# Kernel tuning notes

Hardware: AMD Instinct MI355X
Metric: run time of the kernel (lower is better)

Reference implementation:

```python
import jax, jax.numpy as jnp
import numpy as np

B, L, D = 2, 2048, 1024
H = 16
HD = D // H  # 64


def setup_inputs() -> dict:
    key = jax.random.key(0)
    ks = jax.random.split(key, 7)
    s = 0.02
    return {
        "x": jax.random.normal(ks[0], (B, L, D), dtype=jnp.float32),
        "Wq": jax.random.normal(ks[1], (D, D), dtype=jnp.float32) * s,
        "bq": jnp.zeros((D,), dtype=jnp.float32),
        "Wkv": jax.random.normal(ks[2], (D, 2 * D), dtype=jnp.float32) * s,
        "bkv": jnp.zeros((2 * D,), dtype=jnp.float32),
        "Wo": jax.random.normal(ks[3], (D, D), dtype=jnp.float32) * s,
        "bo": jnp.zeros((D,), dtype=jnp.float32),
    }


def reference(x, Wq, bq, Wkv, bkv, Wo, bo):
    # q/kv projections (self-attention: key/value come from x)
    q = x @ Wq + bq                      # [B, L, D]
    kv = x @ Wkv + bkv                   # [B, L, 2D]
    k, v = jnp.split(kv, 2, axis=-1)     # each [B, L, D]
    # split heads: 'b l (h c) -> b h l c' (rope_embed_fraction=0 -> RoPE is identity)
    def heads(t):
        return t.reshape(B, L, H, HD).transpose(0, 2, 1, 3)
    qh, kh, vh = heads(q), heads(k), heads(v)   # [B, H, L, HD]
    scale = 1.0 / jnp.sqrt(jnp.asarray(HD, dtype=x.dtype))
    scores = jnp.einsum('bhqc,bhkc->bhqk', qh, kh) * scale  # [B, H, L, L]
    attn = jax.nn.softmax(scores, axis=-1)
    y = jnp.einsum('bhqk,bhkc->bhqc', attn, vh)             # [B, H, L, HD]
    # merge heads: 'b h l c -> b l (h c)'
    y = y.transpose(0, 2, 1, 3).reshape(B, L, D)
    return (y @ Wo + bo).reshape(x.shape)
```

## Files before the change

kernel.cpp:

```cpp
#include <hip/hip_runtime.h>

#define B_  2
#define L_  2048
#define D_  1024
#define H_  16
#define HD_ 64

typedef __attribute__((ext_vector_type(8))) short bf16x8;
typedef __attribute__((ext_vector_type(4))) float f32x4;

#define MFMA16(a, b, c) __builtin_amdgcn_mfma_f32_16x16x32_bf16(a, b, c, 0, 0, 0)

__device__ __forceinline__ unsigned short f2bf(float f) {
    union { float f; unsigned u; } v; v.f = f;
    unsigned r = v.u + 0x7FFFu + ((v.u >> 16) & 1u);
    return (unsigned short)(r >> 16);
}

__global__ __launch_bounds__(256) void convert_bf16(
    const float* __restrict__ in, unsigned short* __restrict__ out, int n4)
{
    for (int i = blockIdx.x * blockDim.x + threadIdx.x; i < n4;
         i += gridDim.x * blockDim.x) {
        float4 v = *(const float4*)(in + (size_t)i * 4);
        ushort4 u;
        u.x = f2bf(v.x); u.y = f2bf(v.y); u.z = f2bf(v.z); u.w = f2bf(v.w);
        *(ushort4*)(out + (size_t)i * 4) = u;
    }
}

__global__ __launch_bounds__(256) void prep_w(
    const float* __restrict__ Wq, const float* __restrict__ Wkv,
    const float* __restrict__ Wo,
    unsigned short* __restrict__ Wqt, unsigned short* __restrict__ Wkvt,
    unsigned short* __restrict__ Wot)
{
    __shared__ float t[32][33];
    const int z = blockIdx.z;
    const float* W;  unsigned short* Wt;  int N, nc;
    if (z == 0)      { W = Wq;  Wt = Wqt;  N = 1024; nc = 0; }
    else if (z == 1) { W = Wo;  Wt = Wot;  N = 1024; nc = 0; }
    else             { W = Wkv; Wt = Wkvt; N = 2048; nc = (z - 2) * 1024; }
    const int tx = threadIdx.x & 31, ty = threadIdx.x >> 5;
    const int n0 = nc + blockIdx.x * 32, k0 = blockIdx.y * 32;
    #pragma unroll
    for (int r = 0; r < 4; ++r)
        t[ty + r * 8][tx] = W[(size_t)(k0 + ty + r * 8) * N + n0 + tx];
    __syncthreads();
    #pragma unroll
    for (int r = 0; r < 4; ++r)
        Wt[(size_t)(n0 + ty + r * 8) * 1024 + k0 + tx] = f2bf(t[tx][ty + r * 8]);
}

__global__ __launch_bounds__(512, 1) void gemm_qkv8(
    const unsigned short* __restrict__ A,
    const unsigned short* __restrict__ Bt,
    const float* __restrict__ bq, const float* __restrict__ bkv,
    unsigned short* __restrict__ Qb, unsigned short* __restrict__ Kb,
    unsigned short* __restrict__ Vtg, float qscl)
{
    const int KDIM = 1024, NT = 16;
    __shared__ __align__(16) unsigned short lds[65536];

    const int tid = threadIdx.x;
    const int w = tid >> 6, l = tid & 63, g = l >> 4, ln = l & 15;
    const int wm = (w >> 2) & 1, wn = w & 3;

    const int lin = blockIdx.x;
    const int wg = (lin & 7) * 24 + (lin >> 3);
    const int by = wg / 12, bx = wg % 12;
    const int m0 = by * 256, n0 = bx * 256;

    const int sr8 = w * 8 + (l >> 3);
    const int sc  = (l & 7) ^ ((l >> 3) & 7);
    const unsigned short* Asrc = A  + (size_t)m0 * KDIM + sc * 8;
    const unsigned short* Bsrc = Bt + (size_t)n0 * KDIM + sc * 8;

#define SLOT_A(d, h) (lds + ((d) * 2 + (h)) * 8192)
#define SLOT_B(d, h) (lds + 32768 + ((d) * 2 + (h)) * 8192)

#define STG(slotp, srcp, hh, kt_) do {                                        \
    _Pragma("unroll")                                                         \
    for (int r_ = 0; r_ < 2; ++r_) {                                          \
        const int row_ = (hh) * 128 + r_ * 64 + sr8;                          \
        __builtin_amdgcn_global_load_lds(                                     \
            (const __attribute__((address_space(1))) void*)                   \
                ((srcp) + (size_t)row_ * KDIM + (kt_) * 64),                  \
            (__attribute__((address_space(3))) void*)                         \
                ((slotp) + r_ * 4096 + w * 512 + l * 8),                      \
            16, 0, 0);                                                        \
    }                                                                         \
} while (0)

    f32x4 acc[8][4];
    #pragma unroll
    for (int i = 0; i < 8; ++i)
        #pragma unroll
        for (int j = 0; j < 4; ++j) acc[i][j] = (f32x4){0.f, 0.f, 0.f, 0.f};

    bf16x8 aR[4][2], bB0[2][2], bB1[2][2];

    STG(SLOT_A(0, 0), Asrc, 0, 0);
    STG(SLOT_B(0, 1), Bsrc, 1, 0);
    STG(SLOT_A(0, 1), Asrc, 1, 0);
    STG(SLOT_B(0, 0), Bsrc, 0, 0);
    STG(SLOT_A(1, 0), Asrc, 0, 1);
    STG(SLOT_B(1, 1), Bsrc, 1, 1);

    #pragma unroll 1
    for (int kt = 0; kt < NT; ++kt) {
        const int cur = kt & 1, nxt = cur ^ 1;
        asm volatile("s_waitcnt vmcnt(4)" ::: "memory");
        __builtin_amdgcn_s_barrier();

        #pragma unroll
        for (int mi = 0; mi < 4; ++mi)
            #pragma unroll
            for (int kc = 0; kc < 2; ++kc) {
                const int rho = wm * 64 + mi * 16 + ln, c = kc * 4 + g;
                aR[mi][kc] = *(const bf16x8*)
                    (SLOT_A(cur, 0) + rho * 64 + ((c ^ (rho & 7)) * 8));
            }
        #pragma unroll
        for (int ni = 0; ni < 2; ++ni)
            #pragma unroll
            for (int kc = 0; kc < 2; ++kc) {
                const int rho = wn * 32 + ni * 16 + ln, c = kc * 4 + g;
                bB0[ni][kc] = *(const bf16x8*)
                    (SLOT_B(cur, 0) + rho * 64 + ((c ^ (rho & 7)) * 8));
            }
        if (kt + 1 < NT) STG(SLOT_A(nxt, 1), Asrc, 1, kt + 1);
        __builtin_amdgcn_s_barrier();
        asm volatile("s_waitcnt lgkmcnt(0)" ::: "memory");
        __builtin_amdgcn_s_setprio(1);
        #pragma unroll
        for (int mi = 0; mi < 4; ++mi)
            #pragma unroll
            for (int ni = 0; ni < 2; ++ni) {
                acc[mi][ni] = MFMA16(aR[mi][0], bB0[ni][0], acc[mi][ni]);
                acc[mi][ni] = MFMA16(aR[mi][1], bB0[ni][1], acc[mi][ni]);
            }
        __builtin_amdgcn_s_setprio(0);
        __builtin_amdgcn_s_barrier();

        #pragma unroll
        for (int ni = 0; ni < 2; ++ni)
            #pragma unroll
            for (int kc = 0; kc < 2; ++kc) {
                const int rho = wn * 32 + ni * 16 + ln, c = kc * 4 + g;
                bB1[ni][kc] = *(const bf16x8*)
                    (SLOT_B(cur, 1) + rho * 64 + ((c ^ (rho & 7)) * 8));
            }
        if (kt + 1 < NT) STG(SLOT_B(nxt, 0), Bsrc, 0, kt + 1);
        __builtin_amdgcn_s_barrier();
        asm volatile("s_waitcnt lgkmcnt(0)" ::: "memory");
        __builtin_amdgcn_s_setprio(1);
        #pragma unroll
        for (int mi = 0; mi < 4; ++mi)
            #pragma unroll
            for (int ni = 0; ni < 2; ++ni) {
                acc[mi][2 + ni] = MFMA16(aR[mi][0], bB1[ni][0], acc[mi][2 + ni]);
                acc[mi][2 + ni] = MFMA16(aR[mi][1], bB1[ni][1], acc[mi][2 + ni]);
            }
        __builtin_amdgcn_s_setprio(0);
        __builtin_amdgcn_s_barrier();

        #pragma unroll
        for (int mi = 0; mi < 4; ++mi)
            #pragma unroll
            for (int kc = 0; kc < 2; ++kc) {
                const int rho = wm * 64 + mi * 16 + ln, c = kc * 4 + g;
                aR[mi][kc] = *(const bf16x8*)
                    (SLOT_A(cur, 1) + rho * 64 + ((c ^ (rho & 7)) * 8));
            }
        if (kt + 2 < NT) STG(SLOT_A(cur, 0), Asrc, 0, kt + 2);
        __builtin_amdgcn_s_barrier();
        asm volatile("s_waitcnt lgkmcnt(0)" ::: "memory");
        __builtin_amdgcn_s_setprio(1);
        #pragma unroll
        for (int mi = 0; mi < 4; ++mi)
            #pragma unroll
            for (int ni = 0; ni < 2; ++ni) {
                acc[4 + mi][2 + ni] = MFMA16(aR[mi][0], bB1[ni][0], acc[4 + mi][2 + ni]);
                acc[4 + mi][2 + ni] = MFMA16(aR[mi][1], bB1[ni][1], acc[4 + mi][2 + ni]);
            }
        __builtin_amdgcn_s_setprio(0);
        __builtin_amdgcn_s_barrier();

        if (kt + 2 < NT) STG(SLOT_B(cur, 1), Bsrc, 1, kt + 2);
        __builtin_amdgcn_s_barrier();
        __builtin_amdgcn_s_setprio(1);
        #pragma unroll
        for (int mi = 0; mi < 4; ++mi)
            #pragma unroll
            for (int ni = 0; ni < 2; ++ni) {
                acc[4 + mi][ni] = MFMA16(aR[mi][0], bB0[ni][0], acc[4 + mi][ni]);
                acc[4 + mi][ni] = MFMA16(aR[mi][1], bB0[ni][1], acc[4 + mi][ni]);
            }
        __builtin_amdgcn_s_setprio(0);
        __builtin_amdgcn_s_barrier();
    }
#undef STG
#undef SLOT_A
#undef SLOT_B

    const int region = n0 >> 10;
    if (region == 2) {
        #pragma unroll
        for (int nh = 0; nh < 2; ++nh)
            #pragma unroll
            for (int ni = 0; ni < 2; ++ni) {
                const int d = n0 - 2048 + nh * 128 + wn * 32 + ni * 16 + ln;
                const float bv = bkv[1024 + d];
                #pragma unroll
                for (int mh = 0; mh < 2; ++mh)
                    #pragma unroll
                    for (int mi = 0; mi < 4; ++mi) {
                        const int tok = m0 + mh * 128 + wm * 64 + mi * 16 + g * 4;
                        const int bb = tok >> 11, t4 = tok & 2047;
                        const f32x4 av = acc[mh * 4 + mi][nh * 2 + ni];
                        ushort4 p4;
                        p4.x = f2bf(av[0] + bv); p4.y = f2bf(av[1] + bv);
                        p4.z = f2bf(av[2] + bv); p4.w = f2bf(av[3] + bv);
                        *(ushort4*)(Vtg + ((size_t)bb * 1024 + d) * 2048 + t4) = p4;
                    }
            }
    } else {
        const int isQ = (region == 0);
        const float osc = isQ ? qscl : 1.f;
        #pragma unroll
        for (int nh = 0; nh < 2; ++nh)
            #pragma unroll
            for (int ni = 0; ni < 2; ++ni) {
                const int col = n0 + nh * 128 + wn * 32 + ni * 16 + ln;
                const float bv = isQ ? bq[col] : bkv[col - 1024];
                const int ck = isQ ? col : col - 1024;
                #pragma unroll
                for (int mh = 0; mh < 2; ++mh)
                    #pragma unroll
                    for (int mi = 0; mi < 4; ++mi) {
                        const int row = m0 + mh * 128 + wm * 64 + mi * 16 + g * 4;
                        const f32x4 av = acc[mh * 4 + mi][nh * 2 + ni];
                        #pragma unroll
                        for (int r = 0; r < 4; ++r) {
                            const float vout = (av[r] + bv) * osc;
                            if (isQ)
                                Qb[(size_t)(row + r) * 1024 + ck] = f2bf(vout);
                            else
                                Kb[(size_t)(row + r) * 1024 + ck] = f2bf(vout);
                        }
                    }
            }
    }
}

__global__ __launch_bounds__(256) void gemm_bt(
    const unsigned short* __restrict__ A,
    const unsigned short* __restrict__ Bt,
    const float* __restrict__ bias,
    float* __restrict__ Cout, int M, int N, int K)
{
    __shared__ __align__(16) unsigned short As[128 * 32];
    __shared__ __align__(16) unsigned short Bs[128 * 32];
    const int tid = threadIdx.x;
    const int w = tid >> 6, l = tid & 63, g = l >> 4, ln = l & 15;
    const int wm = w >> 1, wn = w & 1;
    const int m0 = blockIdx.y * 128, n0 = blockIdx.x * 128;

    f32x4 acc[4][4];
    #pragma unroll
    for (int i = 0; i < 4; ++i)
        #pragma unroll
        for (int j = 0; j < 4; ++j) acc[i][j] = (f32x4){0.f, 0.f, 0.f, 0.f};

    const char* Ab = (const char*)A;
    const char* Bb = (const char*)Bt;
    const size_t strideK = (size_t)K * 2;

    for (int k0 = 0; k0 < K; k0 += 32) {
        #pragma unroll
        for (int i = 0; i < 2; ++i) {
            const int b = w * 2048 + i * 1024 + l * 16;
            const int row = b >> 6, cb = b & 63;
            __builtin_amdgcn_global_load_lds(
                (const __attribute__((address_space(1))) void*)
                    (Ab + (size_t)(m0 + row) * strideK + (size_t)k0 * 2 + cb),
                (__attribute__((address_space(3))) void*)
                    ((char*)As + w * 2048 + i * 1024),
                16, 0, 0);
            __builtin_amdgcn_global_load_lds(
                (const __attribute__((address_space(1))) void*)
                    (Bb + (size_t)(n0 + row) * strideK + (size_t)k0 * 2 + cb),
                (__attribute__((address_space(3))) void*)
                    ((char*)Bs + w * 2048 + i * 1024),
                16, 0, 0);
        }
        __syncthreads();
        bf16x8 af[4], bfr[4];
        #pragma unroll
        for (int m = 0; m < 4; ++m)
            af[m] = *(const bf16x8*)(As + (wm * 64 + m * 16 + ln) * 32 + g * 8);
        #pragma unroll
        for (int n = 0; n < 4; ++n)
            bfr[n] = *(const bf16x8*)(Bs + (wn * 64 + n * 16 + ln) * 32 + g * 8);
        #pragma unroll
        for (int m = 0; m < 4; ++m)
            #pragma unroll
            for (int n = 0; n < 4; ++n)
                acc[m][n] = MFMA16(af[m], bfr[n], acc[m][n]);
        __syncthreads();
    }

    #pragma unroll
    for (int n = 0; n < 4; ++n) {
        const int col = n0 + wn * 64 + n * 16 + ln;
        const float bv = bias[col];
        #pragma unroll
        for (int m = 0; m < 4; ++m) {
            const int row = m0 + wm * 64 + m * 16 + g * 4;
            #pragma unroll
            for (int r = 0; r < 4; ++r)
                Cout[(size_t)(row + r) * N + col] = acc[m][n][r] + bv;
        }
    }
}

__global__ __launch_bounds__(256) void attn_mfma(
    const unsigned short* __restrict__ Qb,
    const unsigned short* __restrict__ Kb,
    const unsigned short* __restrict__ Vtg,
    unsigned short* __restrict__ Yb)
{
    __shared__ __align__(16) unsigned short Ks[2][64 * 64];
    __shared__ __align__(16) unsigned short Vs[2][64 * 64];
    __shared__ __align__(16) unsigned short Pl[4][32 * 64];

    const int tid = threadIdx.x;
    const int w = tid >> 6, l = tid & 63, g = l >> 4, ln = l & 15;
    const int dd = blockIdx.x;
    const int bid = (dd & 7) * 64 + (dd >> 3);
    const int qc = bid & 15, h = (bid >> 4) & 15, b = bid >> 8;
    const int qrow = b * L_ + qc * 128 + w * 32;

    const int sub = l >> 3;
    const int scc = (l & 7) ^ sub;
    const unsigned short* ksrc = Kb  + (size_t)(b * L_) * 1024 + h * HD_ + scc * 8;
    const unsigned short* vsrc = Vtg + (size_t)(b * D_ + h * HD_) * 2048 + scc * 8;

#define STAGE(jj, bb) do {                                                    \
    _Pragma("unroll")                                                         \
    for (int i_ = 0; i_ < 2; ++i_) {                                          \
        const int rowK = w * 16 + i_ * 8 + sub;                               \
        __builtin_amdgcn_global_load_lds(                                     \
            (const __attribute__((address_space(1))) void*)                   \
                (ksrc + (size_t)((jj) * 64 + rowK) * 1024),                   \
            (__attribute__((address_space(3))) void*)                         \
                (&Ks[bb][w * 1024 + i_ * 512]), 16, 0, 0);                    \
        __builtin_amdgcn_global_load_lds(                                     \
            (const __attribute__((address_space(1))) void*)                   \
                (vsrc + (size_t)rowK * 2048 + (jj) * 64),                     \
            (__attribute__((address_space(3))) void*)                         \
                (&Vs[bb][w * 1024 + i_ * 512]), 16, 0, 0);                    \
    }                                                                         \
} while (0)

    bf16x8 qa[2][2];
    #pragma unroll
    for (int qt = 0; qt < 2; ++qt)
        #pragma unroll
        for (int c = 0; c < 2; ++c)
            qa[qt][c] = *(const bf16x8*)
                (Qb + (size_t)(qrow + qt * 16 + ln) * D_ + h * HD_ + c * 32 + g * 8);

    f32x4 o[2][4], lacc[2];
    #pragma unroll
    for (int qt = 0; qt < 2; ++qt) {
        #pragma unroll
        for (int dt = 0; dt < 4; ++dt) o[qt][dt] = (f32x4){0.f, 0.f, 0.f, 0.f};
        lacc[qt] = (f32x4){0.f, 0.f, 0.f, 0.f};
    }
    const short one_s = (short)0x3F80;
    const bf16x8 ones = {one_s, one_s, one_s, one_s, one_s, one_s, one_s, one_s};

    unsigned short* Pw = &Pl[w][0];
    const int swzl = (ln & 7) << 3;
    const int swp  = (ln & 7) << 1;

#define ATT_BODY(BUF, TNEXT, NBUF, DOSTG) do {                                \
    if (DOSTG) STAGE(TNEXT, NBUF);                                            \
    const unsigned short* Kc = &Ks[BUF][0];                                   \
    const unsigned short* Vc = &Vs[BUF][0];                                   \
    bf16x8 kb[4][2];                                                          \
    _Pragma("unroll")                                                         \
    for (int kt = 0; kt < 4; ++kt)                                            \
        _Pragma("unroll")                                                     \
        for (int c = 0; c < 2; ++c)                                           \
            kb[kt][c] = *(const bf16x8*)                                      \
                (Kc + (kt * 16 + ln) * 64 + ((c * 32 + g * 8) ^ swzl));       \
    f32x4 s[2][4];                                                            \
    const f32x4 z = (f32x4){0.f, 0.f, 0.f, 0.f};                              \
    __builtin_amdgcn_s_setprio(1);                                            \
    _Pragma("unroll")                                                         \
    for (int qt = 0; qt < 2; ++qt)                                            \
        _Pragma("unroll")                                                     \
        for (int kt = 0; kt < 4; ++kt) {                                      \
            f32x4 t0 = MFMA16(kb[kt][0], qa[qt][0], z);                       \
            s[qt][kt] = MFMA16(kb[kt][1], qa[qt][1], t0);                     \
        }                                                                     \
    __builtin_amdgcn_s_setprio(0);                                            \
    _Pragma("unroll")                                                         \
    for (int qt = 0; qt < 2; ++qt) {                                          \
        const int prow = (qt * 16 + ln) * 64;                                 \
        _Pragma("unroll")                                                     \
        for (int kt = 0; kt < 4; ++kt) {                                      \
            union { float f; unsigned u; } c0, c1, c2u, c3;                   \
            c0.f = __builtin_exp2f(s[qt][kt][0]);                             \
            c1.f = __builtin_exp2f(s[qt][kt][1]);                             \
            c2u.f = __builtin_exp2f(s[qt][kt][2]);                            \
            c3.f = __builtin_exp2f(s[qt][kt][3]);                             \
            uint2 pk;                                                         \
            pk.x = __builtin_amdgcn_perm(c1.u, c0.u, 0x07060302u);            \
            pk.y = __builtin_amdgcn_perm(c3.u, c2u.u, 0x07060302u);           \
            *(uint2*)(Pw + prow + (((kt * 4 + g) ^ swp) << 2)) = pk;          \
        }                                                                     \
    }                                                                         \
    bf16x8 pa[2][2], vb[4][2];                                                \
    _Pragma("unroll")                                                         \
    for (int qt = 0; qt < 2; ++qt)                                            \
        _Pragma("unroll")                                                     \
        for (int c2 = 0; c2 < 2; ++c2)                                        \
            pa[qt][c2] = *(const bf16x8*)                                     \
                (Pw + (qt * 16 + ln) * 64 + (((c2 * 8 + g * 2) ^ swp) << 2)); \
    _Pragma("unroll")                                                         \
    for (int dt = 0; dt < 4; ++dt)                                            \
        _Pragma("unroll")                                                     \
        for (int c2 = 0; c2 < 2; ++c2)                                        \
            vb[dt][c2] = *(const bf16x8*)                                     \
                (Vc + (dt * 16 + ln) * 64 + ((c2 * 32 + g * 8) ^ swzl));      \
    __builtin_amdgcn_s_setprio(1);                                            \
    _Pragma("unroll")                                                         \
    for (int qt = 0; qt < 2; ++qt) {                                          \
        lacc[qt] = MFMA16(pa[qt][0], ones, lacc[qt]);                         \
        lacc[qt] = MFMA16(pa[qt][1], ones, lacc[qt]);                         \
        _Pragma("unroll")                                                     \
        for (int dt = 0; dt < 4; ++dt) {                                      \
            o[qt][dt] = MFMA16(pa[qt][0], vb[dt][0], o[qt][dt]);              \
            o[qt][dt] = MFMA16(pa[qt][1], vb[dt][1], o[qt][dt]);              \
        }                                                                     \
    }                                                                         \
    __builtin_amdgcn_s_setprio(0);                                            \
} while (0)

    STAGE(0, 0);
    __syncthreads();

    #pragma unroll 1
    for (int t = 0; t < L_ / 64; t += 2) {
        ATT_BODY(0, t + 1, 1, true);
        __syncthreads();
        ATT_BODY(1, t + 2, 0, (t + 2 < L_ / 64));
        __syncthreads();
    }
#undef ATT_BODY
#undef STAGE

    #pragma unroll
    for (int qt = 0; qt < 2; ++qt)
        #pragma unroll
        for (int r = 0; r < 4; ++r) {
            const float inv = 1.f / lacc[qt][r];
            const int row = qrow + qt * 16 + g * 4 + r;
            #pragma unroll
            for (int dt = 0; dt < 4; ++dt)
                Yb[(size_t)row * D_ + h * HD_ + dt * 16 + ln] =
                    f2bf(o[qt][dt][r] * inv);
        }
}

extern "C" void kernel_launch(void* const* d_in, const int* in_sizes, int n_in,
                              void* d_out, int out_size, void* d_ws, size_t ws_size,
                              hipStream_t stream)
{
    const float* x   = (const float*)d_in[0];
    const float* Wq  = (const float*)d_in[1];
    const float* bq  = (const float*)d_in[2];
    const float* Wkv = (const float*)d_in[3];
    const float* bkv = (const float*)d_in[4];
    const float* Wo  = (const float*)d_in[5];
    const float* bo  = (const float*)d_in[6];
    float* out = (float*)d_out;

    const int M = B_ * L_;
    unsigned short* ws = (unsigned short*)d_ws;
    unsigned short* xb   = ws;
    unsigned short* Wqt  = xb   + (size_t)M * D_;
    unsigned short* Wkvt = Wqt  + (size_t)D_ * D_;
    unsigned short* Wot  = Wkvt + (size_t)2 * D_ * D_;
    unsigned short* Qb   = Wot  + (size_t)D_ * D_;
    unsigned short* Kb   = Qb   + (size_t)M * D_;
    unsigned short* Vtg  = Kb   + (size_t)M * D_;
    unsigned short* Yb   = Vtg  + (size_t)B_ * D_ * L_;

    const float QSCL = 0.125f * 1.44269504089f;

    convert_bf16<<<2048, 256, 0, stream>>>(x, xb, M * D_ / 4);
    prep_w<<<dim3(32, 32, 4), 256, 0, stream>>>(Wq, Wkv, Wo, Wqt, Wkvt, Wot);

    gemm_qkv8<<<dim3(192), 512, 0, stream>>>(xb, Wqt, bq, bkv, Qb, Kb, Vtg, QSCL);

    attn_mfma<<<dim3(B_ * H_ * (L_ / 128)), 256, 0, stream>>>(Qb, Kb, Vtg, Yb);

    gemm_bt<<<dim3(D_ / 128, M / 128), 256, 0, stream>>>(Yb, Wot, bo, out, M, D_, D_);
}
```

Before: 136.6 us.

## Switch attention to 32x32x16 MFMA and keep P in registers via permlane32 swap

Rewrites the attention inner loop to use 32x32x16 bf16 MFMA tiles instead of 16x16x32, so each wave computes a 32x64 score tile with fewer, larger instructions. The exponentiated scores are packed to bf16 and rearranged into the A-operand layout with v_permlane32_swap, which removes the per-wave LDS scratch buffer for P and its store/load round trip. This lowers LDS traffic and footprint. It relies on the register layouts of the larger MFMA matching the swizzled K/V reads and the permlane shuffle.

```diff
diff --git a/kernel.cpp b/kernel.cpp
--- a/kernel.cpp
+++ b/kernel.cpp
@@ -8,13 +8,20 @@
 
 typedef __attribute__((ext_vector_type(8))) short bf16x8;
 typedef __attribute__((ext_vector_type(4))) float f32x4;
+typedef __attribute__((ext_vector_type(16))) float f32x16;
 
 #define MFMA16(a, b, c) __builtin_amdgcn_mfma_f32_16x16x32_bf16(a, b, c, 0, 0, 0)
+#define MFMA32(a, b, c) __builtin_amdgcn_mfma_f32_32x32x16_bf16(a, b, c, 0, 0, 0)
 
 __device__ __forceinline__ unsigned short f2bf(float f) {
     union { float f; unsigned u; } v; v.f = f;
     unsigned r = v.u + 0x7FFFu + ((v.u >> 16) & 1u);
     return (unsigned short)(r >> 16);
+}
+
+__device__ __forceinline__ unsigned pkbf(float a, float b) {
+    union { float f; unsigned u; } x, y; x.f = a; y.f = b;
+    return __builtin_amdgcn_perm(y.u, x.u, 0x07060302u);
 }
 
 __global__ __launch_bounds__(256) void convert_bf16(
@@ -333,10 +340,10 @@
 {
     __shared__ __align__(16) unsigned short Ks[2][64 * 64];
     __shared__ __align__(16) unsigned short Vs[2][64 * 64];
-    __shared__ __align__(16) unsigned short Pl[4][32 * 64];
 
     const int tid = threadIdx.x;
-    const int w = tid >> 6, l = tid & 63, g = l >> 4, ln = l & 15;
+    const int w = tid >> 6, l = tid & 63;
+    const int l31 = l & 31, hi = l >> 5, l7 = l & 7;
     const int dd = blockIdx.x;
     const int bid = (dd & 7) * 64 + (dd >> 3);
     const int qc = bid & 15, h = (bid >> 4) & 15, b = bid >> 8;
@@ -364,90 +371,81 @@
     }                                                                         \
 } while (0)
 
-    bf16x8 qa[2][2];
-    #pragma unroll
-    for (int qt = 0; qt < 2; ++qt)
-        #pragma unroll
-        for (int c = 0; c < 2; ++c)
-            qa[qt][c] = *(const bf16x8*)
-                (Qb + (size_t)(qrow + qt * 16 + ln) * D_ + h * HD_ + c * 32 + g * 8);
-
-    f32x4 o[2][4], lacc[2];
-    #pragma unroll
-    for (int qt = 0; qt < 2; ++qt) {
-        #pragma unroll
-        for (int dt = 0; dt < 4; ++dt) o[qt][dt] = (f32x4){0.f, 0.f, 0.f, 0.f};
-        lacc[qt] = (f32x4){0.f, 0.f, 0.f, 0.f};
-    }
+    bf16x8 qa[4];
+    #pragma unroll
+    for (int dh = 0; dh < 4; ++dh)
+        qa[dh] = *(const bf16x8*)
+            (Qb + (size_t)(qrow + l31) * D_ + h * HD_ + dh * 16 + hi * 8);
+
+    const f32x16 z16 = {0.f,0.f,0.f,0.f,0.f,0.f,0.f,0.f,
+                        0.f,0.f,0.f,0.f,0.f,0.f,0.f,0.f};
+    f32x16 o2[2], lacc;
+    o2[0] = z16; o2[1] = z16; lacc = z16;
+
     const short one_s = (short)0x3F80;
     const bf16x8 ones = {one_s, one_s, one_s, one_s, one_s, one_s, one_s, one_s};
-
-    unsigned short* Pw = &Pl[w][0];
-    const int swzl = (ln & 7) << 3;
-    const int swp  = (ln & 7) << 1;
 
 #define ATT_BODY(BUF, TNEXT, NBUF, DOSTG) do {                                \
     if (DOSTG) STAGE(TNEXT, NBUF);                                            \
     const unsigned short* Kc = &Ks[BUF][0];                                   \
     const unsigned short* Vc = &Vs[BUF][0];                                   \
-    bf16x8 kb[4][2];                                                          \
-    _Pragma("unroll")                                                         \
-    for (int kt = 0; kt < 4; ++kt)                                            \
+          \
+    bf16x8 kbf[2][4];                                                         \
+    _Pragma("unroll")                                                         \
+    for (int kk = 0; kk < 2; ++kk)                                            \
         _Pragma("unroll")                                                     \
-        for (int c = 0; c < 2; ++c)                                           \
-            kb[kt][c] = *(const bf16x8*)                                      \
-                (Kc + (kt * 16 + ln) * 64 + ((c * 32 + g * 8) ^ swzl));       \
-    f32x4 s[2][4];                                                            \
-    const f32x4 z = (f32x4){0.f, 0.f, 0.f, 0.f};                              \
+        for (int dh = 0; dh < 4; ++dh)                                        \
+            kbf[kk][dh] = *(const bf16x8*)                                    \
+                (Kc + (kk * 32 + l31) * 64 + (((2 * dh + hi) ^ l7) * 8));     \
+    f32x16 s2[2];                                                             \
     __builtin_amdgcn_s_setprio(1);                                            \
     _Pragma("unroll")                                                         \
-    for (int qt = 0; qt < 2; ++qt)                                            \
+    for (int kk = 0; kk < 2; ++kk) {                                          \
+        s2[kk] = MFMA32(kbf[kk][0], qa[0], z16);                              \
+        s2[kk] = MFMA32(kbf[kk][1], qa[1], s2[kk]);                           \
+        s2[kk] = MFMA32(kbf[kk][2], qa[2], s2[kk]);                           \
+        s2[kk] = MFMA32(kbf[kk][3], qa[3], s2[kk]);                           \
+    }                                                                         \
+    __builtin_amdgcn_s_setprio(0);                                            \
+                                                    \
+    _Pragma("unroll")                                                         \
+    for (int kk = 0; kk < 2; ++kk)                                            \
         _Pragma("unroll")                                                     \
-        for (int kt = 0; kt < 4; ++kt) {                                      \
-            f32x4 t0 = MFMA16(kb[kt][0], qa[qt][0], z);                       \
-            s[qt][kt] = MFMA16(kb[kt][1], qa[qt][1], t0);                     \
-        }                                                                     \
-    __builtin_amdgcn_s_setprio(0);                                            \
-    _Pragma("unroll")                                                         \
-    for (int qt = 0; qt < 2; ++qt) {                                          \
-        const int prow = (qt * 16 + ln) * 64;                                 \
+        for (int r = 0; r < 16; ++r)                                          \
+            s2[kk][r] = __builtin_exp2f(s2[kk][r]);                           \
+      \
+    bf16x8 pa[4];                                                             \
+    _Pragma("unroll")                                                         \
+    for (int ks = 0; ks < 4; ++ks) {                                          \
+        const int kk = ks >> 1, R = 8 * (ks & 1);                             \
+        unsigned d0 = pkbf(s2[kk][R + 0], s2[kk][R + 1]);                     \
+        unsigned d1 = pkbf(s2[kk][R + 2], s2[kk][R + 3]);                     \
+        unsigned d2 = pkbf(s2[kk][R + 4], s2[kk][R + 5]);                     \
+        unsigned d3 = pkbf(s2[kk][R + 6], s2[kk][R + 7]);                     \
+               \
+        asm volatile("v_permlane32_swap_b32 %0, %1" : "+v"(d0), "+v"(d2));    \
+        asm volatile("v_permlane32_swap_b32 %0, %1" : "+v"(d1), "+v"(d3));    \
+        union { unsigned u[4]; bf16x8 v; } pk_;                               \
+        pk_.u[0] = d0; pk_.u[1] = d1; pk_.u[2] = d2; pk_.u[3] = d3;           \
+        pa[ks] = pk_.v;                                                       \
+    }                                                                         \
+            \
+    bf16x8 vbf[2][4];                                                         \
+    _Pragma("unroll")                                                         \
+    for (int dt = 0; dt < 2; ++dt)                                            \
         _Pragma("unroll")                                                     \
-        for (int kt = 0; kt < 4; ++kt) {                                      \
-            union { float f; unsigned u; } c0, c1, c2u, c3;                   \
-            c0.f = __builtin_exp2f(s[qt][kt][0]);                             \
-            c1.f = __builtin_exp2f(s[qt][kt][1]);                             \
-            c2u.f = __builtin_exp2f(s[qt][kt][2]);                            \
-            c3.f = __builtin_exp2f(s[qt][kt][3]);                             \
-            uint2 pk;                                                         \
-            pk.x = __builtin_amdgcn_perm(c1.u, c0.u, 0x07060302u);            \
-            pk.y = __builtin_amdgcn_perm(c3.u, c2u.u, 0x07060302u);           \
-            *(uint2*)(Pw + prow + (((kt * 4 + g) ^ swp) << 2)) = pk;          \
-        }                                                                     \
-    }                                                                         \
-    bf16x8 pa[2][2], vb[4][2];                                                \
-    _Pragma("unroll")                                                         \
-    for (int qt = 0; qt < 2; ++qt)                                            \
+        for (int ks = 0; ks < 4; ++ks)                                        \
+            vbf[dt][ks] = *(const bf16x8*)                                    \
+                (Vc + (dt * 32 + l31) * 64 + (((2 * ks + hi) ^ l7) * 8));     \
+    __builtin_amdgcn_s_setprio(1);                                            \
+    _Pragma("unroll")                                                         \
+    for (int dt = 0; dt < 2; ++dt)                                            \
         _Pragma("unroll")                                                     \
-        for (int c2 = 0; c2 < 2; ++c2)                                        \
-            pa[qt][c2] = *(const bf16x8*)                                     \
-                (Pw + (qt * 16 + ln) * 64 + (((c2 * 8 + g * 2) ^ swp) << 2)); \
-    _Pragma("unroll")                                                         \
-    for (int dt = 0; dt < 4; ++dt)                                            \
-        _Pragma("unroll")                                                     \
-        for (int c2 = 0; c2 < 2; ++c2)                                        \
-            vb[dt][c2] = *(const bf16x8*)                                     \
-                (Vc + (dt * 16 + ln) * 64 + ((c2 * 32 + g * 8) ^ swzl));      \
-    __builtin_amdgcn_s_setprio(1);                                            \
-    _Pragma("unroll")                                                         \
-    for (int qt = 0; qt < 2; ++qt) {                                          \
-        lacc[qt] = MFMA16(pa[qt][0], ones, lacc[qt]);                         \
-        lacc[qt] = MFMA16(pa[qt][1], ones, lacc[qt]);                         \
-        _Pragma("unroll")                                                     \
-        for (int dt = 0; dt < 4; ++dt) {                                      \
-            o[qt][dt] = MFMA16(pa[qt][0], vb[dt][0], o[qt][dt]);              \
-            o[qt][dt] = MFMA16(pa[qt][1], vb[dt][1], o[qt][dt]);              \
-        }                                                                     \
-    }                                                                         \
+        for (int ks = 0; ks < 4; ++ks)                                        \
+            o2[dt] = MFMA32(pa[ks], vbf[dt][ks], o2[dt]);                     \
+    _Pragma("unroll")                                                         \
+    for (int ks = 0; ks < 4; ++ks)                                            \
+        lacc = MFMA32(pa[ks], ones, lacc);                                    \
     __builtin_amdgcn_s_setprio(0);                                            \
 } while (0)
 
@@ -465,16 +463,14 @@
 #undef STAGE
 
     #pragma unroll
-    for (int qt = 0; qt < 2; ++qt)
-        #pragma unroll
-        for (int r = 0; r < 4; ++r) {
-            const float inv = 1.f / lacc[qt][r];
-            const int row = qrow + qt * 16 + g * 4 + r;
-            #pragma unroll
-            for (int dt = 0; dt < 4; ++dt)
-                Yb[(size_t)row * D_ + h * HD_ + dt * 16 + ln] =
-                    f2bf(o[qt][dt][r] * inv);
-        }
+    for (int r = 0; r < 16; ++r) {
+        const float inv = 1.f / lacc[r];
+        const int row = qrow + (r & 3) + 8 * (r >> 2) + 4 * hi;
+        #pragma unroll
+        for (int dt = 0; dt < 2; ++dt)
+            Yb[(size_t)row * D_ + h * HD_ + dt * 32 + l31] =
+                f2bf(o2[dt][r] * inv);
+    }
 }
 
 extern "C" void kernel_launch(void* const* d_in, const int* in_sizes, int n_in,
```

Result: no change. 137.9 us (+1.0%).
